# Kernel optimization log

Hardware: AMD Instinct MI355X
Metric: run time of the kernel (lower is better)

The kernel has to match this reference:

```python
import jax, jax.numpy as jnp
import numpy as np

B, S, HID = 4, 2048, 512
NH, HD = 8, 64          # num heads, head dim (num_kv_heads == NH, so GQA group = 1)
SW = 250                # sliding window
THETA = 10000.0
SCALING = 1.0 / np.sqrt(HD)
NEG_INF = jnp.finfo(jnp.float32).min


def setup_inputs() -> dict:
    key = jax.random.key(0)
    ks = jax.random.split(key, 5)
    w_std = 1.0 / np.sqrt(HID)
    return {
        "hidden_states": jax.random.normal(ks[0], (B, S, HID), jnp.float32),
        "position_ids": jnp.broadcast_to(jnp.arange(S, dtype=jnp.int64), (B, S)),
        "Wq": jax.random.normal(ks[1], (NH * HD, HID), jnp.float32) * w_std,
        "Wk": jax.random.normal(ks[2], (NH * HD, HID), jnp.float32) * w_std,
        "Wv": jax.random.normal(ks[3], (NH * HD, HID), jnp.float32) * w_std,
        "Wo": jax.random.normal(ks[4], (HID, NH * HD), jnp.float32) * w_std,
    }


def _rotate_half(x):
    x1, x2 = jnp.split(x, 2, axis=-1)
    return jnp.concatenate((-x2, x1), axis=-1)


def reference(hidden_states, position_ids, Wq, Wk, Wv, Wo):
    b, s, _ = hidden_states.shape
    dtype = hidden_states.dtype

    # QKV projections (Linear: x @ W.T, no bias) -> [b, h, s, d]
    q = (hidden_states @ Wq.T).reshape(b, s, NH, HD).transpose(0, 2, 1, 3)
    k = (hidden_states @ Wk.T).reshape(b, s, NH, HD).transpose(0, 2, 1, 3)
    v = (hidden_states @ Wv.T).reshape(b, s, NH, HD).transpose(0, 2, 1, 3)

    # Rotary embedding (MimiRotaryEmbedding), computed in fp32
    inv_freq = 1.0 / (THETA ** (jnp.arange(0, HD, 2, dtype=jnp.float32) / HD))
    freqs = position_ids.astype(jnp.float32)[:, :, None] * inv_freq[None, None, :]  # [b, s, HD/2]
    emb = jnp.concatenate((freqs, freqs), axis=-1)                                   # [b, s, HD]
    cos = jnp.cos(emb).astype(dtype)[:, None, :, :]  # unsqueeze head dim
    sin = jnp.sin(emb).astype(dtype)[:, None, :, :]
    q = q * cos + _rotate_half(q) * sin
    k = k * cos + _rotate_half(k) * sin

    # Sliding-window causal additive mask: keep kv iff q_idx >= kv_idx and q_idx - kv_idx <= SW
    idx = jnp.arange(s)
    keep = (idx[:, None] >= idx[None, :]) & ((idx[:, None] - idx[None, :]) <= SW)
    bias = jnp.where(keep, 0.0, NEG_INF).astype(jnp.float32)  # [s, s]

    # Eager attention: full scores, fp32 softmax (num_key_value_groups == 1)
    scores = jnp.einsum("bhqd,bhkd->bhqk", q, k) * SCALING
    scores = scores.astype(jnp.float32) + bias[None, None, :, :]
    attn = jax.nn.softmax(scores, axis=-1).astype(dtype)
    out = jnp.einsum("bhqk,bhkd->bhqd", attn, v)

    # merge heads and output projection
    out = out.transpose(0, 2, 1, 3).reshape(b, s, NH * HD)
    return out @ Wo.T
```

## Files before the change

### kernel.cpp

```cpp
#include <hip/hip_runtime.h>
#include <hip/hip_bf16.h>
#include <math.h>


#define B_   4
#define S_   2048
#define HID_ 512
#define NH_  8
#define HD_  64
#define SW_  250

typedef __bf16 bf16x8 __attribute__((ext_vector_type(8)));
typedef __bf16 bf16x4 __attribute__((ext_vector_type(4)));
typedef float f32x4 __attribute__((ext_vector_type(4)));
using bf16_t = __hip_bfloat16;
typedef unsigned int u32;

__device__ __forceinline__ void glds16(const void* g, void* l) {
    __builtin_amdgcn_global_load_lds(
        (const __attribute__((address_space(1))) u32*)g,
        (__attribute__((address_space(3))) u32*)l, 16, 0, 0);
}

__global__ __launch_bounds__(256) void cvt_all(
    const float* __restrict__ X,  const float* __restrict__ Wq,
    const float* __restrict__ Wk, const float* __restrict__ Wv,
    const float* __restrict__ Wo,
    bf16_t* __restrict__ Xb, bf16_t* __restrict__ Wcat, bf16_t* __restrict__ Wob)
{
    const int blk = blockIdx.x;
    const float* s; bf16_t* d; size_t base;
    if (blk < 2048)      { s = X;  d = Xb;            base = (size_t)blk * 2048; }
    else if (blk < 2176) { s = Wq; d = Wcat;          base = (size_t)(blk - 2048) * 2048; }
    else if (blk < 2304) { s = Wk; d = Wcat + 262144; base = (size_t)(blk - 2176) * 2048; }
    else if (blk < 2432) { s = Wv; d = Wcat + 524288; base = (size_t)(blk - 2304) * 2048; }
    else                 { s = Wo; d = Wob;           base = (size_t)(blk - 2432) * 2048; }
    size_t i = base + (size_t)threadIdx.x * 8;
    float4 a = *reinterpret_cast<const float4*>(s + i);
    float4 b = *reinterpret_cast<const float4*>(s + i + 4);
    bf16x8 r;
    r[0] = (__bf16)a.x; r[1] = (__bf16)a.y; r[2] = (__bf16)a.z; r[3] = (__bf16)a.w;
    r[4] = (__bf16)b.x; r[5] = (__bf16)b.y; r[6] = (__bf16)b.z; r[7] = (__bf16)b.w;
    *reinterpret_cast<bf16x8*>(d + i) = r;
}

__global__ __launch_bounds__(256) void qkv_gemm(
    const bf16_t* __restrict__ Xb, const bf16_t* __restrict__ Wcat,
    bf16_t* __restrict__ Q, bf16_t* __restrict__ Kbuf, bf16_t* __restrict__ Vt)
{
    __shared__ __align__(16) char smem_raw[34816];
    bf16_t* As = (bf16_t*)smem_raw;
    bf16_t* Bs = As + 4096;
    const int tid = threadIdx.x;
    const int wave = tid >> 6, lane = tid & 63;
    const int quad = lane >> 4, l16 = lane & 15;
    const int wm = wave & 1, wn = wave >> 1;

    const int g = blockIdx.x;
    const int xcd = g & 7, slot = g >> 3;
    const int mi = xcd * 8 + (slot & 7);
    const int ni = slot >> 3;
    const int m0 = mi * 128, n0 = ni * 128;

    f32x4 acc[4][4] = {};
    for (int k0 = 0; k0 < HID_; k0 += 32) {
#pragma unroll
        for (int rr = 0; rr < 2; ++rr) {
            int slot2 = rr * 256 + tid;
            int row = slot2 >> 2;
            int l = (slot2 & 3) ^ ((row >> 1) & 3);
            glds16(Xb + (size_t)(m0 + row) * HID_ + k0 + l * 8, As + slot2 * 8);
            glds16(Wcat + (size_t)(n0 + row) * HID_ + k0 + l * 8, Bs + slot2 * 8);
        }
        __syncthreads();
        bf16x8 af[4], bfr[4];
#pragma unroll
        for (int i = 0; i < 4; ++i) {
            int ra = wm * 64 + i * 16 + l16;
            int rb = wn * 64 + i * 16 + l16;
            int pa = quad ^ ((ra >> 1) & 3);
            int pb = quad ^ ((rb >> 1) & 3);
            af[i]  = *reinterpret_cast<const bf16x8*>(&As[ra * 32 + pa * 8]);
            bfr[i] = *reinterpret_cast<const bf16x8*>(&Bs[rb * 32 + pb * 8]);
        }
#pragma unroll
        for (int mi2 = 0; mi2 < 4; ++mi2)
#pragma unroll
            for (int ni2 = 0; ni2 < 4; ++ni2)
                acc[mi2][ni2] = __builtin_amdgcn_mfma_f32_16x16x32_bf16(af[mi2], bfr[ni2], acc[mi2][ni2], 0, 0, 0);
        __syncthreads();
    }

    const int seg = n0 >> 9;
    const int hh = ((n0 & 511) + wn * 64) >> 6;
    bf16_t* wt = (bf16_t*)smem_raw + wave * 4352;
    const int mbase = m0 + wm * 64;
    const int bb = mbase >> 11;
    const int sbase = mbase & (S_ - 1);

    if (seg < 2) {
        const float qs = (seg == 0) ? 0.125f : 1.0f;
        const float c = 0.41524101186f;
        float inv0 = exp2f(-(float)l16 * c);
        float inv1 = exp2f(-(float)(l16 + 16) * c);
#pragma unroll
        for (int mi2 = 0; mi2 < 4; ++mi2)
#pragma unroll
            for (int r = 0; r < 4; ++r) {
                int lrow = mi2 * 16 + quad * 4 + r;
                float sf = (float)(sbase + lrow);
#pragma unroll
                for (int ip = 0; ip < 2; ++ip) {
                    float sn, cs_;
                    __sincosf(sf * (ip ? inv1 : inv0), &sn, &cs_);
                    float x1 = acc[mi2][ip][r], x2 = acc[mi2][ip + 2][r];
                    wt[lrow * 68 + ip * 16 + l16]      = __float2bfloat16((x1 * cs_ - x2 * sn) * qs);
                    wt[lrow * 68 + ip * 16 + l16 + 32] = __float2bfloat16((x2 * cs_ + x1 * sn) * qs);
                }
            }
        bf16_t* Y = (seg == 0) ? Q : Kbuf;
#pragma unroll
        for (int it = 0; it < 8; ++it) {
            int e = it * 64 + lane;
            int sr = e >> 3, doff = (e & 7) * 8;
            size_t g2 = ((size_t)(bb * NH_ + hh) * S_ + sbase + sr) * HD_ + doff;
            *reinterpret_cast<bf16x8*>(Y + g2) =
                *reinterpret_cast<const bf16x8*>(wt + sr * 68 + doff);
        }
    } else {
#pragma unroll
        for (int mi2 = 0; mi2 < 4; ++mi2)
#pragma unroll
            for (int ni2 = 0; ni2 < 4; ++ni2)
#pragma unroll
                for (int r = 0; r < 4; ++r)
                    wt[(ni2 * 16 + l16) * 68 + mi2 * 16 + quad * 4 + r] =
                        __float2bfloat16(acc[mi2][ni2][r]);
#pragma unroll
        for (int it = 0; it < 8; ++it) {
            int e = it * 64 + lane;
            int d = e >> 3, soff = (e & 7) * 8;
            size_t g2 = ((size_t)(bb * NH_ + hh) * HD_ + d) * S_ + sbase + soff;
            *reinterpret_cast<bf16x8*>(Vt + g2) =
                *reinterpret_cast<const bf16x8*>(wt + d * 68 + soff);
        }
    }
}

__global__ __launch_bounds__(256) void attn_mfma(
    const bf16_t* __restrict__ Q, const bf16_t* __restrict__ K,
    const bf16_t* __restrict__ Vt, bf16_t* __restrict__ A)
{
    __shared__ __align__(16) __bf16 Ks[2][32 * 64];
    __shared__ __align__(16) __bf16 Vs[2][64 * 32];
    __shared__ __align__(16) __bf16 pt[4][16][40];
    __shared__ float sums_l[4][16];
    const int tid = threadIdx.x;
    const int wave = tid >> 6, lane = tid & 63;
    const int quad = lane >> 4, l16 = lane & 15;

    const int g = blockIdx.x;
    const int xcd = g & 7, slot = g >> 3;
    const int bh = xcd * 4 + (slot >> 5);
    const int qt = slot & 31;
    const int b = bh >> 3, h = bh & 7;
    const int q0b = qt * 64;
    const int q0 = q0b + wave * 16;

    const size_t bh_  = (size_t)(b * NH_ + h) * S_;
    const size_t bhd = (size_t)(b * NH_ + h) * HD_;

    bf16x8 qf0, qf1;
    {
        const bf16_t* qp = Q + (bh_ + q0 + l16) * HD_ + quad * 8;
        qf0 = *reinterpret_cast<const bf16x8*>(qp);
        qf1 = *reinterpret_cast<const bf16x8*>(qp + 32);
    }
    const int kstartB = (q0b > SW_) ? ((q0b - SW_) & ~31) : 0;
    const int ntB = (q0b + 95 - kstartB) >> 5;
    const int qq = q0 + l16;

    const int krow = tid >> 3, kl = (tid & 7) ^ (krow & 7);
    const int vrow = tid >> 2, vl = (tid & 3) ^ (vrow & 3);

    {
        const int kb = kstartB;
        glds16(K  + (bh_ + kb + krow) * HD_ + kl * 8, &Ks[0][tid * 8]);
        glds16(Vt + (bhd + vrow) * S_ + kb + vl * 8, &Vs[0][tid * 8]);
    }

    float sum = 0.f;
    f32x4 o[4] = {};
    for (int t = 0; t < ntB; ++t) {
        const int cur = t & 1;
        const int kb = kstartB + t * 32;
        if (t + 1 < ntB) {
            const int kb2 = kb + 32;
            glds16(K  + (bh_ + kb2 + krow) * HD_ + kl * 8, &Ks[cur ^ 1][tid * 8]);
            glds16(Vt + (bhd + vrow) * S_ + kb2 + vl * 8, &Vs[cur ^ 1][tid * 8]);
            asm volatile("s_waitcnt vmcnt(2)" ::: "memory");
        } else {
            asm volatile("s_waitcnt vmcnt(0)" ::: "memory");
        }
        __builtin_amdgcn_s_barrier();
        asm volatile("" ::: "memory");

#pragma unroll
        for (int half = 0; half < 2; ++half) {
            const int rowt = half * 16 + l16;
            const int p0 = quad ^ (rowt & 7);
            const int p1 = (quad ^ 4) ^ (rowt & 7);
            bf16x8 k0 = *reinterpret_cast<const bf16x8*>(&Ks[cur][rowt * 64 + p0 * 8]);
            bf16x8 k1 = *reinterpret_cast<const bf16x8*>(&Ks[cur][rowt * 64 + p1 * 8]);
            f32x4 z = {};
            z = __builtin_amdgcn_mfma_f32_16x16x32_bf16(k0, qf0, z, 0, 0, 0);
            z = __builtin_amdgcn_mfma_f32_16x16x32_bf16(k1, qf1, z, 0, 0, 0);
            const int kbase = kb + half * 16 + quad * 4;
            bf16x4 pk;
#pragma unroll
            for (int r = 0; r < 4; ++r) {
                int key = kbase + r;
                bool keep = (key <= qq) && (qq - key <= SW_);
                float p = keep ? __expf(z[r]) : 0.f;
                sum += p;
                pk[r] = (__bf16)p;
            }
            *reinterpret_cast<bf16x4*>(&pt[wave][l16][half * 16 + quad * 4]) = pk;
        }
        bf16x8 pf = *reinterpret_cast<const bf16x8*>(&pt[wave][l16][quad * 8]);
#pragma unroll
        for (int nf = 0; nf < 4; ++nf) {
            const int rowv = nf * 16 + l16;
            const int pv = quad ^ (rowv & 3);
            bf16x8 vf = *reinterpret_cast<const bf16x8*>(&Vs[cur][rowv * 32 + pv * 8]);
            o[nf] = __builtin_amdgcn_mfma_f32_16x16x32_bf16(pf, vf, o[nf], 0, 0, 0);
        }
        asm volatile("" ::: "memory");
        __builtin_amdgcn_s_barrier();
        asm volatile("" ::: "memory");
    }

    sum += __shfl_xor(sum, 16, 64);
    sum += __shfl_xor(sum, 32, 64);
    if (quad == 0) sums_l[wave][l16] = sum;
    float inv_l[4];
#pragma unroll
    for (int r = 0; r < 4; ++r) inv_l[r] = 1.0f / sums_l[wave][quad * 4 + r];
#pragma unroll
    for (int nf = 0; nf < 4; ++nf)
#pragma unroll
        for (int r = 0; r < 4; ++r) {
            int qr = q0 + quad * 4 + r;
            A[((size_t)(b * S_ + qr)) * HID_ + h * HD_ + nf * 16 + l16] =
                __float2bfloat16(o[nf][r] * inv_l[r]);
        }
}

__global__ __launch_bounds__(256) void out_proj(
    const bf16_t* __restrict__ Ain, const bf16_t* __restrict__ Wob,
    float* __restrict__ out)
{
    __shared__ __align__(16) bf16_t As[128 * 32];
    __shared__ __align__(16) bf16_t Bs[64 * 32];
    const int tid = threadIdx.x;
    const int wave = tid >> 6, lane = tid & 63;
    const int quad = lane >> 4, l16 = lane & 15;
    const int m0 = blockIdx.x * 128, n0 = blockIdx.y * 64;

    f32x4 acc[2][4] = {};
    for (int k0 = 0; k0 < HID_; k0 += 32) {
#pragma unroll
        for (int rr = 0; rr < 2; ++rr) {
            int slot = rr * 256 + tid;
            int row = slot >> 2;
            int l = (slot & 3) ^ ((row >> 1) & 3);
            glds16(Ain + (size_t)(m0 + row) * HID_ + k0 + l * 8, As + slot * 8);
        }
        {
            int slot = tid;
            int row = slot >> 2;
            int l = (slot & 3) ^ ((row >> 1) & 3);
            glds16(Wob + (size_t)(n0 + row) * HID_ + k0 + l * 8, Bs + slot * 8);
        }
        __syncthreads();
        bf16x8 af[2], bfr[4];
#pragma unroll
        for (int i = 0; i < 2; ++i) {
            int ra = wave * 32 + i * 16 + l16;
            int pa = quad ^ ((ra >> 1) & 3);
            af[i] = *reinterpret_cast<const bf16x8*>(&As[ra * 32 + pa * 8]);
        }
#pragma unroll
        for (int i = 0; i < 4; ++i) {
            int rb = i * 16 + l16;
            int pb = quad ^ ((rb >> 1) & 3);
            bfr[i] = *reinterpret_cast<const bf16x8*>(&Bs[rb * 32 + pb * 8]);
        }
#pragma unroll
        for (int mi = 0; mi < 2; ++mi)
#pragma unroll
            for (int ni = 0; ni < 4; ++ni)
                acc[mi][ni] = __builtin_amdgcn_mfma_f32_16x16x32_bf16(af[mi], bfr[ni], acc[mi][ni], 0, 0, 0);
        __syncthreads();
    }
#pragma unroll
    for (int mi = 0; mi < 2; ++mi)
#pragma unroll
        for (int ni = 0; ni < 4; ++ni)
#pragma unroll
            for (int r = 0; r < 4; ++r) {
                int m = m0 + wave * 32 + mi * 16 + quad * 4 + r;
                int n = n0 + ni * 16 + l16;
                out[(size_t)m * HID_ + n] = acc[mi][ni][r];
            }
}

extern "C" void kernel_launch(void* const* d_in, const int* in_sizes, int n_in,
                              void* d_out, int out_size, void* d_ws, size_t ws_size,
                              hipStream_t stream)
{
    const float* X  = (const float*)d_in[0];
    const float* Wq = (const float*)d_in[2];
    const float* Wk = (const float*)d_in[3];
    const float* Wv = (const float*)d_in[4];
    const float* Wo = (const float*)d_in[5];

    char* ws = (char*)d_ws;
    const size_t elems = (size_t)B_ * NH_ * S_ * HD_;
    const size_t wsz   = (size_t)HID_ * HID_;
    bf16_t* Q    = (bf16_t*)ws;
    bf16_t* K    = Q + elems;
    bf16_t* Vt   = K + elems;
    bf16_t* Xb   = Vt + elems;
    bf16_t* A    = Xb;
    bf16_t* Wcat = Xb + elems;
    bf16_t* Wob  = Wcat + 3 * wsz;

    cvt_all<<<2560, 256, 0, stream>>>(X, Wq, Wk, Wv, Wo, Xb, Wcat, Wob);
    qkv_gemm<<<768, 256, 0, stream>>>(Xb, Wcat, Q, K, Vt);
    attn_mfma<<<1024, 256, 0, stream>>>(Q, K, Vt, A);
    out_proj<<<dim3(64, 8), 256, 0, stream>>>(A, Wob, (float*)d_out);
}
```

Before: 125.9 us.

## Double-buffer QKV GEMM LDS tiles with async global-to-LDS prefetch

Restructures the QKV projection GEMM main loop to double-buffer the A and B tiles in shared memory. It prefetches the next k-slice with global_load_lds before computing on the current one, and uses explicit vmcnt waits plus raw s_barrier instead of __syncthreads. The goal is to hide global load latency behind the MFMA work. Shared memory use stays within the existing 34816-byte buffer, since two tiles take 32KB. The explicit waitcnt counting depends on the exact number of outstanding loads.

```diff
diff --git a/kernel.cpp b/kernel.cpp
--- a/kernel.cpp
+++ b/kernel.cpp
@@ -49,8 +49,7 @@
     bf16_t* __restrict__ Q, bf16_t* __restrict__ Kbuf, bf16_t* __restrict__ Vt)
 {
     __shared__ __align__(16) char smem_raw[34816];
-    bf16_t* As = (bf16_t*)smem_raw;
-    bf16_t* Bs = As + 4096;
+    bf16_t* const sm = (bf16_t*)smem_raw;
     const int tid = threadIdx.x;
     const int wave = tid >> 6, lane = tid & 63;
     const int quad = lane >> 4, l16 = lane & 15;
@@ -62,17 +61,33 @@
     const int ni = slot >> 3;
     const int m0 = mi * 128, n0 = ni * 128;
 
+    const int srow0 = tid >> 2,           sl0 = (tid & 3) ^ ((srow0 >> 1) & 3);
+    const int srow1 = (256 + tid) >> 2,   sl1 = ((256 + tid) & 3) ^ ((srow1 >> 1) & 3);
+
+    glds16(Xb   + (size_t)(m0 + srow0) * HID_ + sl0 * 8, sm + tid * 8);
+    glds16(Wcat + (size_t)(n0 + srow0) * HID_ + sl0 * 8, sm + 4096 + tid * 8);
+    glds16(Xb   + (size_t)(m0 + srow1) * HID_ + sl1 * 8, sm + (256 + tid) * 8);
+    glds16(Wcat + (size_t)(n0 + srow1) * HID_ + sl1 * 8, sm + 4096 + (256 + tid) * 8);
+
     f32x4 acc[4][4] = {};
-    for (int k0 = 0; k0 < HID_; k0 += 32) {
-#pragma unroll
-        for (int rr = 0; rr < 2; ++rr) {
-            int slot2 = rr * 256 + tid;
-            int row = slot2 >> 2;
-            int l = (slot2 & 3) ^ ((row >> 1) & 3);
-            glds16(Xb + (size_t)(m0 + row) * HID_ + k0 + l * 8, As + slot2 * 8);
-            glds16(Wcat + (size_t)(n0 + row) * HID_ + k0 + l * 8, Bs + slot2 * 8);
-        }
-        __syncthreads();
+    for (int t = 0; t < 16; ++t) {
+        const int curo = (t & 1) * 8192;
+        if (t + 1 < 16) {
+            const int nxto = curo ^ 8192;
+            const int k1 = (t + 1) * 32;
+            glds16(Xb   + (size_t)(m0 + srow0) * HID_ + k1 + sl0 * 8, sm + nxto + tid * 8);
+            glds16(Wcat + (size_t)(n0 + srow0) * HID_ + k1 + sl0 * 8, sm + nxto + 4096 + tid * 8);
+            glds16(Xb   + (size_t)(m0 + srow1) * HID_ + k1 + sl1 * 8, sm + nxto + (256 + tid) * 8);
+            glds16(Wcat + (size_t)(n0 + srow1) * HID_ + k1 + sl1 * 8, sm + nxto + 4096 + (256 + tid) * 8);
+            asm volatile("s_waitcnt vmcnt(4)" ::: "memory");
+        } else {
+            asm volatile("s_waitcnt vmcnt(0)" ::: "memory");
+        }
+        __builtin_amdgcn_sched_barrier(0);
+        __builtin_amdgcn_s_barrier();
+        __builtin_amdgcn_sched_barrier(0);
+        asm volatile("" ::: "memory");
+
         bf16x8 af[4], bfr[4];
 #pragma unroll
         for (int i = 0; i < 4; ++i) {
@@ -80,20 +95,24 @@
             int rb = wn * 64 + i * 16 + l16;
             int pa = quad ^ ((ra >> 1) & 3);
             int pb = quad ^ ((rb >> 1) & 3);
-            af[i]  = *reinterpret_cast<const bf16x8*>(&As[ra * 32 + pa * 8]);
-            bfr[i] = *reinterpret_cast<const bf16x8*>(&Bs[rb * 32 + pb * 8]);
+            af[i]  = *reinterpret_cast<const bf16x8*>(sm + curo + ra * 32 + pa * 8);
+            bfr[i] = *reinterpret_cast<const bf16x8*>(sm + curo + 4096 + rb * 32 + pb * 8);
         }
 #pragma unroll
         for (int mi2 = 0; mi2 < 4; ++mi2)
 #pragma unroll
             for (int ni2 = 0; ni2 < 4; ++ni2)
                 acc[mi2][ni2] = __builtin_amdgcn_mfma_f32_16x16x32_bf16(af[mi2], bfr[ni2], acc[mi2][ni2], 0, 0, 0);
-        __syncthreads();
+        asm volatile("" ::: "memory");
+        __builtin_amdgcn_sched_barrier(0);
+        __builtin_amdgcn_s_barrier();
+        __builtin_amdgcn_sched_barrier(0);
+        asm volatile("" ::: "memory");
     }
 
     const int seg = n0 >> 9;
     const int hh = ((n0 & 511) + wn * 64) >> 6;
-    bf16_t* wt = (bf16_t*)smem_raw + wave * 4352;
+    bf16_t* wt = sm + wave * 4352;
     const int mbase = m0 + wm * 64;
     const int bb = mbase >> 11;
     const int sbase = mbase & (S_ - 1);
```

Result: no change. 125.6 us (-0.3%).

## Fuse fp32-to-bf16 conversion into QKV and output projection GEMM loads

Applied to the files above, without the earlier changes.

Removes the standalone conversion kernel and loads fp32 activations and weights directly in the QKV and output-projection GEMMs. Values are converted to bf16 in registers and stored into swizzled LDS, with register double-buffered prefetch of the next K slice. This avoids a full extra pass writing and rereading bf16 copies plus one launch. The cost is that GEMM tiles now read fp32 data, which doubles global/L2 traffic per tile, and async global-to-LDS loads are replaced by register staging.

```diff
diff --git a/kernel.cpp b/kernel.cpp
--- a/kernel.cpp
+++ b/kernel.cpp
@@ -22,35 +22,22 @@
         (__attribute__((address_space(3))) u32*)l, 16, 0, 0);
 }
 
-__global__ __launch_bounds__(256) void cvt_all(
-    const float* __restrict__ X,  const float* __restrict__ Wq,
-    const float* __restrict__ Wk, const float* __restrict__ Wv,
-    const float* __restrict__ Wo,
-    bf16_t* __restrict__ Xb, bf16_t* __restrict__ Wcat, bf16_t* __restrict__ Wob)
-{
-    const int blk = blockIdx.x;
-    const float* s; bf16_t* d; size_t base;
-    if (blk < 2048)      { s = X;  d = Xb;            base = (size_t)blk * 2048; }
-    else if (blk < 2176) { s = Wq; d = Wcat;          base = (size_t)(blk - 2048) * 2048; }
-    else if (blk < 2304) { s = Wk; d = Wcat + 262144; base = (size_t)(blk - 2176) * 2048; }
-    else if (blk < 2432) { s = Wv; d = Wcat + 524288; base = (size_t)(blk - 2304) * 2048; }
-    else                 { s = Wo; d = Wob;           base = (size_t)(blk - 2432) * 2048; }
-    size_t i = base + (size_t)threadIdx.x * 8;
-    float4 a = *reinterpret_cast<const float4*>(s + i);
-    float4 b = *reinterpret_cast<const float4*>(s + i + 4);
+__device__ __forceinline__ bf16x8 cvt8(float4 a, float4 b) {
     bf16x8 r;
     r[0] = (__bf16)a.x; r[1] = (__bf16)a.y; r[2] = (__bf16)a.z; r[3] = (__bf16)a.w;
     r[4] = (__bf16)b.x; r[5] = (__bf16)b.y; r[6] = (__bf16)b.z; r[7] = (__bf16)b.w;
-    *reinterpret_cast<bf16x8*>(d + i) = r;
+    return r;
 }
 
 __global__ __launch_bounds__(256) void qkv_gemm(
-    const bf16_t* __restrict__ Xb, const bf16_t* __restrict__ Wcat,
+    const float* __restrict__ X,  const float* __restrict__ Wq,
+    const float* __restrict__ Wk, const float* __restrict__ Wv,
     bf16_t* __restrict__ Q, bf16_t* __restrict__ Kbuf, bf16_t* __restrict__ Vt)
 {
     __shared__ __align__(16) char smem_raw[34816];
-    bf16_t* As = (bf16_t*)smem_raw;
-    bf16_t* Bs = As + 4096;
+    bf16_t* const sm = (bf16_t*)smem_raw;
+    bf16_t* const As = sm;
+    bf16_t* const Bs = sm + 4096;
     const int tid = threadIdx.x;
     const int wave = tid >> 6, lane = tid & 63;
     const int quad = lane >> 4, l16 = lane & 15;
@@ -62,17 +49,45 @@
     const int ni = slot >> 3;
     const int m0 = mi * 128, n0 = ni * 128;
 
+    const int srow = tid >> 1, shalf = tid & 1;
+    const int swz = (srow >> 1) & 3;
+    const int pc0 = ((shalf * 2) ^ swz) * 8;
+    const int pc1 = ((shalf * 2 + 1) ^ swz) * 8;
+    const int seg = n0 >> 9;
+    const float* Wsel = (seg == 0) ? Wq : (seg == 1) ? Wk : Wv;
+    const float* xrow = X    + (size_t)(m0 + srow) * HID_ + shalf * 16;
+    const float* wrow = Wsel + (size_t)((n0 & 511) + srow) * HID_ + shalf * 16;
+
+    float4 a0, a1, a2, a3, b0, b1, b2, b3;
+    a0 = *reinterpret_cast<const float4*>(xrow + 0);
+    a1 = *reinterpret_cast<const float4*>(xrow + 4);
+    a2 = *reinterpret_cast<const float4*>(xrow + 8);
+    a3 = *reinterpret_cast<const float4*>(xrow + 12);
+    b0 = *reinterpret_cast<const float4*>(wrow + 0);
+    b1 = *reinterpret_cast<const float4*>(wrow + 4);
+    b2 = *reinterpret_cast<const float4*>(wrow + 8);
+    b3 = *reinterpret_cast<const float4*>(wrow + 12);
+
     f32x4 acc[4][4] = {};
-    for (int k0 = 0; k0 < HID_; k0 += 32) {
-#pragma unroll
-        for (int rr = 0; rr < 2; ++rr) {
-            int slot2 = rr * 256 + tid;
-            int row = slot2 >> 2;
-            int l = (slot2 & 3) ^ ((row >> 1) & 3);
-            glds16(Xb + (size_t)(m0 + row) * HID_ + k0 + l * 8, As + slot2 * 8);
-            glds16(Wcat + (size_t)(n0 + row) * HID_ + k0 + l * 8, Bs + slot2 * 8);
-        }
+    for (int t = 0; t < 16; ++t) {
+        float4 na0, na1, na2, na3, nb0, nb1, nb2, nb3;
+        if (t + 1 < 16) {
+            const int k1 = (t + 1) * 32;
+            na0 = *reinterpret_cast<const float4*>(xrow + k1 + 0);
+            na1 = *reinterpret_cast<const float4*>(xrow + k1 + 4);
+            na2 = *reinterpret_cast<const float4*>(xrow + k1 + 8);
+            na3 = *reinterpret_cast<const float4*>(xrow + k1 + 12);
+            nb0 = *reinterpret_cast<const float4*>(wrow + k1 + 0);
+            nb1 = *reinterpret_cast<const float4*>(wrow + k1 + 4);
+            nb2 = *reinterpret_cast<const float4*>(wrow + k1 + 8);
+            nb3 = *reinterpret_cast<const float4*>(wrow + k1 + 12);
+        }
+        *reinterpret_cast<bf16x8*>(&As[srow * 32 + pc0]) = cvt8(a0, a1);
+        *reinterpret_cast<bf16x8*>(&As[srow * 32 + pc1]) = cvt8(a2, a3);
+        *reinterpret_cast<bf16x8*>(&Bs[srow * 32 + pc0]) = cvt8(b0, b1);
+        *reinterpret_cast<bf16x8*>(&Bs[srow * 32 + pc1]) = cvt8(b2, b3);
         __syncthreads();
+
         bf16x8 af[4], bfr[4];
 #pragma unroll
         for (int i = 0; i < 4; ++i) {
@@ -89,11 +104,12 @@
             for (int ni2 = 0; ni2 < 4; ++ni2)
                 acc[mi2][ni2] = __builtin_amdgcn_mfma_f32_16x16x32_bf16(af[mi2], bfr[ni2], acc[mi2][ni2], 0, 0, 0);
         __syncthreads();
-    }
-
-    const int seg = n0 >> 9;
+        a0 = na0; a1 = na1; a2 = na2; a3 = na3;
+        b0 = nb0; b1 = nb1; b2 = nb2; b3 = nb3;
+    }
+
     const int hh = ((n0 & 511) + wn * 64) >> 6;
-    bf16_t* wt = (bf16_t*)smem_raw + wave * 4352;
+    bf16_t* wt = sm + wave * 4352;
     const int mbase = m0 + wm * 64;
     const int bb = mbase >> 11;
     const int sbase = mbase & (S_ - 1);
@@ -257,7 +273,7 @@
 }
 
 __global__ __launch_bounds__(256) void out_proj(
-    const bf16_t* __restrict__ Ain, const bf16_t* __restrict__ Wob,
+    const bf16_t* __restrict__ Ain, const float* __restrict__ Wo,
     float* __restrict__ out)
 {
     __shared__ __align__(16) bf16_t As[128 * 32];
@@ -267,8 +283,17 @@
     const int quad = lane >> 4, l16 = lane & 15;
     const int m0 = blockIdx.x * 128, n0 = blockIdx.y * 64;
 
+    const int brow = tid >> 2, bchunk = tid & 3;
+    const int bpc = (bchunk ^ ((brow >> 1) & 3)) * 8;
+    const float* worow = Wo + (size_t)(n0 + brow) * HID_ + bchunk * 8;
+
+    float4 cb0, cb1;
+    cb0 = *reinterpret_cast<const float4*>(worow + 0);
+    cb1 = *reinterpret_cast<const float4*>(worow + 4);
+
     f32x4 acc[2][4] = {};
-    for (int k0 = 0; k0 < HID_; k0 += 32) {
+    for (int t = 0; t < 16; ++t) {
+        const int k0 = t * 32;
 #pragma unroll
         for (int rr = 0; rr < 2; ++rr) {
             int slot = rr * 256 + tid;
@@ -276,13 +301,15 @@
             int l = (slot & 3) ^ ((row >> 1) & 3);
             glds16(Ain + (size_t)(m0 + row) * HID_ + k0 + l * 8, As + slot * 8);
         }
-        {
-            int slot = tid;
-            int row = slot >> 2;
-            int l = (slot & 3) ^ ((row >> 1) & 3);
-            glds16(Wob + (size_t)(n0 + row) * HID_ + k0 + l * 8, Bs + slot * 8);
-        }
+        float4 nb0, nb1;
+        if (t + 1 < 16) {
+            const int k1 = (t + 1) * 32;
+            nb0 = *reinterpret_cast<const float4*>(worow + k1 + 0);
+            nb1 = *reinterpret_cast<const float4*>(worow + k1 + 4);
+        }
+        *reinterpret_cast<bf16x8*>(&Bs[brow * 32 + bpc]) = cvt8(cb0, cb1);
         __syncthreads();
+
         bf16x8 af[2], bfr[4];
 #pragma unroll
         for (int i = 0; i < 2; ++i) {
@@ -302,6 +329,7 @@
             for (int ni = 0; ni < 4; ++ni)
                 acc[mi][ni] = __builtin_amdgcn_mfma_f32_16x16x32_bf16(af[mi], bfr[ni], acc[mi][ni], 0, 0, 0);
         __syncthreads();
+        cb0 = nb0; cb1 = nb1;
     }
 #pragma unroll
     for (int mi = 0; mi < 2; ++mi)
@@ -327,17 +355,12 @@
 
     char* ws = (char*)d_ws;
     const size_t elems = (size_t)B_ * NH_ * S_ * HD_;
-    const size_t wsz   = (size_t)HID_ * HID_;
-    bf16_t* Q    = (bf16_t*)ws;
-    bf16_t* K    = Q + elems;
-    bf16_t* Vt   = K + elems;
-    bf16_t* Xb   = Vt + elems;
-    bf16_t* A    = Xb;
-    bf16_t* Wcat = Xb + elems;
-    bf16_t* Wob  = Wcat + 3 * wsz;
-
-    cvt_all<<<2560, 256, 0, stream>>>(X, Wq, Wk, Wv, Wo, Xb, Wcat, Wob);
-    qkv_gemm<<<768, 256, 0, stream>>>(Xb, Wcat, Q, K, Vt);
+    bf16_t* Q  = (bf16_t*)ws;
+    bf16_t* K  = Q + elems;
+    bf16_t* Vt = K + elems;
+    bf16_t* A  = Vt + elems;
+
+    qkv_gemm<<<768, 256, 0, stream>>>(X, Wq, Wk, Wv, Q, K, Vt);
     attn_mfma<<<1024, 256, 0, stream>>>(Q, K, Vt, A);
-    out_proj<<<dim3(64, 8), 256, 0, stream>>>(A, Wob, (float*)d_out);
-}
+    out_proj<<<dim3(64, 8), 256, 0, stream>>>(A, Wo, (float*)d_out);
+}
```

Measured after the change: 134.7 us. 1.07x slower.
